# Kernel tuning notes

Hardware: AMD Instinct MI355X
Metric: run time of the kernel (lower is better)

The kernel has to match this reference:

```python
import jax, jax.numpy as jnp
import numpy as np

SFREQ = 256.0
BANDS = [(0.5, 4.0), (4.0, 8.0), (8.0, 13.0), (13.0, 30.0), (30.0, 50.0)]


def setup_inputs() -> dict:
    key = jax.random.key(0)
    k0, k1, k2 = jax.random.split(key, 3)
    B, T, C, D = 32, 4096, 64, 512
    n_bands = len(BANDS)
    x = jax.random.normal(k0, (B, T, C), dtype=jnp.float32)
    W1 = jax.random.normal(k1, (C * n_bands, D // 2), dtype=jnp.float32) * 0.05
    b1 = jnp.zeros((D // 2,), dtype=jnp.float32)
    W2 = jax.random.normal(k2, (D // 2, D), dtype=jnp.float32) * 0.05
    b2 = jnp.zeros((D,), dtype=jnp.float32)
    return {"x": x, "W1": W1, "b1": b1, "W2": W2, "b2": b2}


def reference(x, W1, b1, W2, b2):
    B, T, C = x.shape
    W = min(int(SFREQ), T)          # window size
    hop = W // 2
    # Static window start indices (overlapping STFT windows)
    starts = np.arange(0, T - W + 1, hop)
    idx = starts[:, None] + np.arange(W)[None, :]            # (nW, W)
    windows = jnp.take(x, jnp.asarray(idx), axis=1)          # (B, nW, W, C)

    # Batched rFFT over the window (time) axis, all windows at once
    xf = jnp.fft.rfft(windows, axis=2)                       # (B, nW, F, C) complex
    power = jnp.abs(xf) ** 2                                  # (B, nW, F, C)

    # Static band masks -> mean over in-band frequency bins (matches masked .mean)
    freqs = np.fft.rfftfreq(W, d=1.0 / SFREQ)
    masks = np.stack([((freqs >= lo) & (freqs <= hi)).astype(np.float32)
                      for lo, hi in BANDS])                   # (5, F)
    masks = masks / masks.sum(axis=1, keepdims=True)
    band = jnp.einsum('bnfc,kf->bnkc', power, jnp.asarray(masks))  # (B, nW, 5, C)
    # torch.cat of per-band (B, C) blocks is band-major -> reshape matches
    feat = band.reshape(B, band.shape[1], -1)                 # (B, nW, 5*C)

    # band_proj MLP
    h = jax.nn.relu(feat @ W1 + b1)
    feat = h @ W2 + b2                                        # (B, nW, D)

    # F.interpolate(mode='linear', align_corners=False) from nW -> T
    nW = feat.shape[1]
    pos = (jnp.arange(T, dtype=jnp.float32) + 0.5) * (nW / T) - 0.5
    pos = jnp.clip(pos, 0.0, float(nW - 1))
    i0 = jnp.floor(pos).astype(jnp.int32)
    i1 = jnp.minimum(i0 + 1, nW - 1)
    w = (pos - i0.astype(jnp.float32))[None, :, None]
    out = feat[:, i0] * (1.0 - w) + feat[:, i1] * w           # (B, T, D)
    return out
```

## Files before the change

### kernel.cpp

```cpp
#include <hip/hip_runtime.h>
#include <hip/hip_bf16.h>
#include <math.h>

#define BB 32
#define TT 4096
#define CC 64
#define DD 512
#define NW 31
#define WIN 256
#define HOP 128
#define NROWS (BB * NW)

typedef float f32x4 __attribute__((ext_vector_type(4)));

__global__ __launch_bounds__(256) void k_bandpower(const float* __restrict__ x,
                                                   float* __restrict__ feat) {
    __shared__ float xs[128 * 64];
    __shared__ float bpart[4][5][64];

    const int tid = threadIdx.x;
    const int c   = tid & 63;
    const int g   = tid >> 6;
    const int blk = blockIdx.x;
    const int b   = blk / NW;
    const int n   = blk % NW;

    for (int i = tid; i < 4 * 5 * 64; i += 256) ((float*)bpart)[i] = 0.0f;

    float coef[13], s1[13], s2[13];
#pragma unroll
    for (int j = 0; j < 13; ++j) {
        const int f = 1 + g + 4 * j;
        coef[j] = 2.0f * cospif((float)f * (1.0f / 128.0f));
        s1[j] = 0.0f;
        s2[j] = 0.0f;
    }

    const size_t winBase = ((size_t)b * TT + (size_t)n * HOP) * CC;

    for (int half = 0; half < 2; ++half) {
        const f32x4* src = (const f32x4*)(x + winBase + (size_t)half * 128 * CC);
        f32x4* dst = (f32x4*)xs;
        for (int i = tid; i < (128 * 64) / 4; i += 256) dst[i] = src[i];
        __syncthreads();

#pragma unroll 4
        for (int tt = 0; tt < 128; ++tt) {
            const float xv = xs[tt * 64 + c];
#pragma unroll
            for (int j = 0; j < 13; ++j) {
                const float sn = fmaf(coef[j], s1[j], xv - s2[j]);
                s2[j] = s1[j];
                s1[j] = sn;
            }
        }
        __syncthreads();
    }

#pragma unroll
    for (int j = 0; j < 13; ++j) {
        const int f = 1 + g + 4 * j;
        if (f > 50) continue;
        const float p = fmaf(s1[j], s1[j],
                        fmaf(s2[j], s2[j], -coef[j] * s1[j] * s2[j]));
        if (f <= 4)             bpart[g][0][c] += p;
        if (f >= 4 && f <= 8)   bpart[g][1][c] += p;
        if (f >= 8 && f <= 13)  bpart[g][2][c] += p;
        if (f >= 13 && f <= 30) bpart[g][3][c] += p;
        if (f >= 30)            bpart[g][4][c] += p;
    }
    __syncthreads();

    const float wband[5] = {1.0f / 4.0f, 1.0f / 5.0f, 1.0f / 6.0f,
                            1.0f / 18.0f, 1.0f / 21.0f};
    for (int idx = tid; idx < 320; idx += 256) {
        const int k  = idx >> 6;
        const int cc = idx & 63;
        float s = bpart[0][k][cc] + bpart[1][k][cc] +
                  bpart[2][k][cc] + bpart[3][k][cc];
        feat[(size_t)blk * 320 + idx] = s * wband[k];
    }
}

__global__ __launch_bounds__(256) void k_mlp(const float* __restrict__ feat,
                                             const float* __restrict__ W1,
                                             const float* __restrict__ b1,
                                             const float* __restrict__ W2,
                                             const float* __restrict__ b2,
                                             float* __restrict__ feat2) {
    __shared__ float fs[4][320];
    __shared__ float hs[4][256];

    const int tid  = threadIdx.x;
    const int row0 = blockIdx.x * 4;

    for (int i = tid; i < 4 * 320; i += 256)
        ((float*)fs)[i] = feat[(size_t)row0 * 320 + i];
    __syncthreads();

    float acc[4];
    {
        const float bias = b1[tid];
#pragma unroll
        for (int r = 0; r < 4; ++r) acc[r] = bias;
        for (int i = 0; i < 320; ++i) {
            const float w = W1[(size_t)i * 256 + tid];
#pragma unroll
            for (int r = 0; r < 4; ++r) acc[r] = fmaf(fs[r][i], w, acc[r]);
        }
#pragma unroll
        for (int r = 0; r < 4; ++r) hs[r][tid] = fmaxf(acc[r], 0.0f);
    }
    __syncthreads();

    float o0[4], o1[4];
    {
        const float bias0 = b2[tid];
        const float bias1 = b2[tid + 256];
#pragma unroll
        for (int r = 0; r < 4; ++r) { o0[r] = bias0; o1[r] = bias1; }
        for (int i = 0; i < 256; ++i) {
            const float w0 = W2[(size_t)i * 512 + tid];
            const float w1 = W2[(size_t)i * 512 + tid + 256];
#pragma unroll
            for (int r = 0; r < 4; ++r) {
                const float h = hs[r][i];
                o0[r] = fmaf(h, w0, o0[r]);
                o1[r] = fmaf(h, w1, o1[r]);
            }
        }
    }
#pragma unroll
    for (int r = 0; r < 4; ++r) {
        feat2[(size_t)(row0 + r) * 512 + tid]       = o0[r];
        feat2[(size_t)(row0 + r) * 512 + tid + 256] = o1[r];
    }
}

__global__ __launch_bounds__(256) void k_interp(const float* __restrict__ feat2,
                                                float* __restrict__ out) {
    const int tid  = threadIdx.x;
    const int bt   = blockIdx.x * 2 + (tid >> 7);
    const int d4   = tid & 127;
    const int t    = bt & (TT - 1);
    const int b    = bt >> 12;

    float pos = ((float)t + 0.5f) * (31.0f / 4096.0f) - 0.5f;
    pos = fminf(fmaxf(pos, 0.0f), 30.0f);
    const int   i0 = (int)pos;
    const int   i1 = min(i0 + 1, 30);
    const float w  = pos - (float)i0;
    const float w0 = 1.0f - w;

    const f32x4* r0 = (const f32x4*)(feat2 + ((size_t)b * NW + i0) * DD);
    const f32x4* r1 = (const f32x4*)(feat2 + ((size_t)b * NW + i1) * DD);
    f32x4* o = (f32x4*)(out + (size_t)bt * DD);

    const f32x4 a  = r0[d4];
    const f32x4 cc = r1[d4];
    f32x4 res = a * w0 + cc * w;
    __builtin_nontemporal_store(res, &o[d4]);
}

extern "C" void kernel_launch(void* const* d_in, const int* in_sizes, int n_in,
                              void* d_out, int out_size, void* d_ws, size_t ws_size,
                              hipStream_t stream) {
    const float* x  = (const float*)d_in[0];
    const float* W1 = (const float*)d_in[1];
    const float* b1 = (const float*)d_in[2];
    const float* W2 = (const float*)d_in[3];
    const float* b2 = (const float*)d_in[4];
    float* out = (float*)d_out;

    float* feat  = (float*)d_ws;
    float* feat2 = feat + (size_t)NROWS * 320;

    k_bandpower<<<NROWS, 256, 0, stream>>>(x, feat);
    k_mlp<<<NROWS / 4, 256, 0, stream>>>(feat, W1, b1, W2, b2, feat2);
    k_interp<<<(BB * TT) / 2, 256, 0, stream>>>(feat2, out);
}
```

Baseline: 116.4 us.

## Fold window halves into even/odd sums for Goertzel and widen MLP row tiles

The bandpower kernel now computes u=a+b and v=a-b from the two 128-sample window halves. Even-frequency bins are then run over 128 samples of u and odd bins over v, which halves the Goertzel recurrence length. Block size doubles to 512 threads, 8 groups with 7 bins each, and per-thread band partials stay in registers before a single LDS reduction. The MLP kernel processes 8 rows per block instead of 4 to reuse each weight load across more rows, at the cost of more registers and fewer blocks (124).

```diff
diff --git a/kernel.cpp b/kernel.cpp
--- a/kernel.cpp
+++ b/kernel.cpp
@@ -13,10 +13,11 @@
 
 typedef float f32x4 __attribute__((ext_vector_type(4)));
 
-__global__ __launch_bounds__(256) void k_bandpower(const float* __restrict__ x,
+__global__ __launch_bounds__(512) void k_bandpower(const float* __restrict__ x,
                                                    float* __restrict__ feat) {
-    __shared__ float xs[128 * 64];
-    __shared__ float bpart[4][5][64];
+    __shared__ float lds[16384];
+    float* u = lds;
+    float* v = lds + 8192;
 
     const int tid = threadIdx.x;
     const int c   = tid & 63;
@@ -25,59 +26,68 @@
     const int b   = blk / NW;
     const int n   = blk % NW;
 
-    for (int i = tid; i < 4 * 5 * 64; i += 256) ((float*)bpart)[i] = 0.0f;
+    const size_t winBase = ((size_t)b * TT + (size_t)n * HOP) * CC;
+    const f32x4* h0 = (const f32x4*)(x + winBase);
+    const f32x4* h1 = (const f32x4*)(x + winBase + 128 * CC);
+    f32x4* u4 = (f32x4*)u;
+    f32x4* v4 = (f32x4*)v;
+    for (int i = tid; i < 2048; i += 512) {
+        const f32x4 a  = h0[i];
+        const f32x4 bb = h1[i];
+        u4[i] = a + bb;
+        v4[i] = a - bb;
+    }
+    __syncthreads();
 
-    float coef[13], s1[13], s2[13];
+    float coef[7], s1[7], s2[7];
 #pragma unroll
-    for (int j = 0; j < 13; ++j) {
-        const int f = 1 + g + 4 * j;
+    for (int j = 0; j < 7; ++j) {
+        const int f = 1 + g + 8 * j;
         coef[j] = 2.0f * cospif((float)f * (1.0f / 128.0f));
         s1[j] = 0.0f;
         s2[j] = 0.0f;
     }
-
-    const size_t winBase = ((size_t)b * TT + (size_t)n * HOP) * CC;
-
-    for (int half = 0; half < 2; ++half) {
-        const f32x4* src = (const f32x4*)(x + winBase + (size_t)half * 128 * CC);
-        f32x4* dst = (f32x4*)xs;
-        for (int i = tid; i < (128 * 64) / 4; i += 256) dst[i] = src[i];
-        __syncthreads();
+    const float* src = ((g & 1) ? u : v) + c;
 
 #pragma unroll 4
-        for (int tt = 0; tt < 128; ++tt) {
-            const float xv = xs[tt * 64 + c];
+    for (int tt = 0; tt < 128; ++tt) {
+        const float xv = src[tt * 64];
 #pragma unroll
-            for (int j = 0; j < 13; ++j) {
-                const float sn = fmaf(coef[j], s1[j], xv - s2[j]);
-                s2[j] = s1[j];
-                s1[j] = sn;
-            }
+        for (int j = 0; j < 7; ++j) {
+            const float sn = fmaf(coef[j], s1[j], xv - s2[j]);
+            s2[j] = s1[j];
+            s1[j] = sn;
         }
-        __syncthreads();
     }
+    __syncthreads();
 
+    float pb[5] = {0.0f, 0.0f, 0.0f, 0.0f, 0.0f};
 #pragma unroll
-    for (int j = 0; j < 13; ++j) {
-        const int f = 1 + g + 4 * j;
+    for (int j = 0; j < 7; ++j) {
+        const int f = 1 + g + 8 * j;
         if (f > 50) continue;
         const float p = fmaf(s1[j], s1[j],
                         fmaf(s2[j], s2[j], -coef[j] * s1[j] * s2[j]));
-        if (f <= 4)             bpart[g][0][c] += p;
-        if (f >= 4 && f <= 8)   bpart[g][1][c] += p;
-        if (f >= 8 && f <= 13)  bpart[g][2][c] += p;
-        if (f >= 13 && f <= 30) bpart[g][3][c] += p;
-        if (f >= 30)            bpart[g][4][c] += p;
+        if (f <= 4)             pb[0] += p;
+        if (f >= 4 && f <= 8)   pb[1] += p;
+        if (f >= 8 && f <= 13)  pb[2] += p;
+        if (f >= 13 && f <= 30) pb[3] += p;
+        if (f >= 30)            pb[4] += p;
     }
+
+    float (*bpart)[5][64] = (float (*)[5][64])lds;
+#pragma unroll
+    for (int k = 0; k < 5; ++k) bpart[g][k][c] = pb[k];
     __syncthreads();
 
     const float wband[5] = {1.0f / 4.0f, 1.0f / 5.0f, 1.0f / 6.0f,
                             1.0f / 18.0f, 1.0f / 21.0f};
-    for (int idx = tid; idx < 320; idx += 256) {
+    for (int idx = tid; idx < 320; idx += 512) {
         const int k  = idx >> 6;
         const int cc = idx & 63;
-        float s = bpart[0][k][cc] + bpart[1][k][cc] +
-                  bpart[2][k][cc] + bpart[3][k][cc];
+        float s = 0.0f;
+#pragma unroll
+        for (int gg = 0; gg < 8; ++gg) s += bpart[gg][k][cc];
         feat[(size_t)blk * 320 + idx] = s * wband[k];
     }
 }
@@ -88,42 +98,42 @@
                                              const float* __restrict__ W2,
                                              const float* __restrict__ b2,
                                              float* __restrict__ feat2) {
-    __shared__ float fs[4][320];
-    __shared__ float hs[4][256];
+    __shared__ float fs[8][320];
+    __shared__ float hs[8][256];
 
     const int tid  = threadIdx.x;
-    const int row0 = blockIdx.x * 4;
+    const int row0 = blockIdx.x * 8;
 
-    for (int i = tid; i < 4 * 320; i += 256)
+    for (int i = tid; i < 8 * 320; i += 256)
         ((float*)fs)[i] = feat[(size_t)row0 * 320 + i];
     __syncthreads();
 
-    float acc[4];
+    float acc[8];
     {
         const float bias = b1[tid];
 #pragma unroll
-        for (int r = 0; r < 4; ++r) acc[r] = bias;
+        for (int r = 0; r < 8; ++r) acc[r] = bias;
         for (int i = 0; i < 320; ++i) {
             const float w = W1[(size_t)i * 256 + tid];
 #pragma unroll
-            for (int r = 0; r < 4; ++r) acc[r] = fmaf(fs[r][i], w, acc[r]);
+            for (int r = 0; r < 8; ++r) acc[r] = fmaf(fs[r][i], w, acc[r]);
         }
 #pragma unroll
-        for (int r = 0; r < 4; ++r) hs[r][tid] = fmaxf(acc[r], 0.0f);
+        for (int r = 0; r < 8; ++r) hs[r][tid] = fmaxf(acc[r], 0.0f);
     }
     __syncthreads();
 
-    float o0[4], o1[4];
+    float o0[8], o1[8];
     {
         const float bias0 = b2[tid];
         const float bias1 = b2[tid + 256];
 #pragma unroll
-        for (int r = 0; r < 4; ++r) { o0[r] = bias0; o1[r] = bias1; }
+        for (int r = 0; r < 8; ++r) { o0[r] = bias0; o1[r] = bias1; }
         for (int i = 0; i < 256; ++i) {
             const float w0 = W2[(size_t)i * 512 + tid];
             const float w1 = W2[(size_t)i * 512 + tid + 256];
 #pragma unroll
-            for (int r = 0; r < 4; ++r) {
+            for (int r = 0; r < 8; ++r) {
                 const float h = hs[r][i];
                 o0[r] = fmaf(h, w0, o0[r]);
                 o1[r] = fmaf(h, w1, o1[r]);
@@ -131,7 +141,7 @@
         }
     }
 #pragma unroll
-    for (int r = 0; r < 4; ++r) {
+    for (int r = 0; r < 8; ++r) {
         feat2[(size_t)(row0 + r) * 512 + tid]       = o0[r];
         feat2[(size_t)(row0 + r) * 512 + tid + 256] = o1[r];
     }
@@ -175,7 +185,7 @@
     float* feat  = (float*)d_ws;
     float* feat2 = feat + (size_t)NROWS * 320;
 
-    k_bandpower<<<NROWS, 256, 0, stream>>>(x, feat);
-    k_mlp<<<NROWS / 4, 256, 0, stream>>>(feat, W1, b1, W2, b2, feat2);
+    k_bandpower<<<NROWS, 512, 0, stream>>>(x, feat);
+    k_mlp<<<NROWS / 8, 256, 0, stream>>>(feat, W1, b1, W2, b2, feat2);
     k_interp<<<(BB * TT) / 2, 256, 0, stream>>>(feat2, out);
 }
```

After: 111.6 us. -4.1%, faster.
